# Kernel optimization log

Measured on AMD Instinct MI355X. Metric: run time of the kernel, lower is better.

Reference implementation:

```python
import jax, jax.numpy as jnp
import numpy as np

D_MODEL = 1024
NUM_HEADS = 16
D_K = D_MODEL // NUM_HEADS
EPS = 1e-12  # F.normalize eps


def setup_inputs() -> dict:
    key = jax.random.key(0)
    ks = jax.random.split(key, 12)
    B, S = 4, 2048
    scale = 1.0 / np.sqrt(D_MODEL)
    inp = {
        'query': jax.random.normal(ks[0], (B, S, D_MODEL), jnp.float32),
        'key': jax.random.normal(ks[1], (B, S, D_MODEL), jnp.float32),
        'value': jax.random.normal(ks[2], (B, S, D_MODEL), jnp.float32),
        'w_q': jax.random.normal(ks[3], (D_MODEL, D_MODEL), jnp.float32) * scale,
        'b_q': jax.random.normal(ks[4], (D_MODEL,), jnp.float32) * scale,
        'w_k': jax.random.normal(ks[5], (D_MODEL, D_MODEL), jnp.float32) * scale,
        'b_k': jax.random.normal(ks[6], (D_MODEL,), jnp.float32) * scale,
        'w_v': jax.random.normal(ks[7], (D_MODEL, D_MODEL), jnp.float32) * scale,
        'b_v': jax.random.normal(ks[8], (D_MODEL,), jnp.float32) * scale,
        'w_o': jax.random.normal(ks[9], (D_MODEL, D_MODEL), jnp.float32) * scale,
        'b_o': jax.random.normal(ks[10], (D_MODEL,), jnp.float32) * scale,
    }
    return inp


def _split_heads(x, B, S):
    # [B,S,D] -> [B,H,S,d_k]
    return x.reshape(B, S, NUM_HEADS, D_K).transpose(0, 2, 1, 3)


def _l2_normalize(x):
    # matches F.normalize(p=2, dim=-1): x / max(||x||, eps)
    n = jnp.sqrt(jnp.sum(x * x, axis=-1, keepdims=True))
    return x / jnp.maximum(n, EPS)


def reference(query, key, value, w_q, b_q, w_k, b_k, w_v, b_v, w_o, b_o):
    B, S, _ = query.shape
    Q = _split_heads(query @ w_q.T + b_q, B, S)
    K = _split_heads(key @ w_k.T + b_k, B, S)
    V = _split_heads(value @ w_v.T + b_v, B, S)
    Qn = _l2_normalize(Q)
    Kn = _l2_normalize(K)
    # cosine similarity clamped to >=1, acosh, exp(-dist)
    sim = jnp.einsum('bhqd,bhkd->bhqk', Qn, Kn)
    dist = jnp.arccosh(jnp.maximum(sim, 1.0))
    w = jnp.exp(-dist)
    out = jnp.einsum('bhqk,bhkd->bhqd', w, V)
    out = out.transpose(0, 2, 1, 3).reshape(B, S, D_MODEL)
    return out @ w_o.T + b_o
```

## Files before the change

### kernel.cpp

```cpp
#include <hip/hip_runtime.h>


constexpr int B = 4;
constexpr int S = 2048;
constexpr int D = 1024;
constexpr int SCHUNK = 32;
constexpr int NCHUNK = S / SCHUNK;

__global__ void k_colsum_partial(const float* __restrict__ value,
                                 float* __restrict__ partial) {
  const int d = blockIdx.x * blockDim.x + threadIdx.x;
  const int c = blockIdx.y;
  const int b = blockIdx.z;
  const float* p = value + (((size_t)b * S) + (size_t)c * SCHUNK) * D + d;
  float acc = 0.f;
#pragma unroll
  for (int i = 0; i < SCHUNK; ++i) acc += p[(size_t)i * D];
  partial[(((size_t)b * NCHUNK) + c) * D + d] = acc;
}

__global__ void k_colsum_reduce(const float* __restrict__ partial,
                                float* __restrict__ vsum) {
  const int d = blockIdx.x * blockDim.x + threadIdx.x;
  const int b = blockIdx.y;
  const float* p = partial + (size_t)b * NCHUNK * D + d;
  float acc = 0.f;
#pragma unroll
  for (int c = 0; c < NCHUNK; ++c) acc += p[(size_t)c * D];
  vsum[(size_t)b * D + d] = acc;
}

__global__ void k_gemv4(const float* __restrict__ x, const float* __restrict__ w,
                        const float* __restrict__ bias, float bias_scale,
                        float* __restrict__ y) {
  const int j = blockIdx.x;
  const int lane = threadIdx.x & 63;
  const int b = threadIdx.x >> 6;
  const float4* wr = (const float4*)(w + (size_t)j * D);
  const float4* xr = (const float4*)(x + (size_t)b * D);
  float acc = 0.f;
#pragma unroll
  for (int i = 0; i < D / 4 / 64; ++i) {
    float4 a = wr[lane + 64 * i];
    float4 c = xr[lane + 64 * i];
    acc += a.x * c.x + a.y * c.y + a.z * c.z + a.w * c.w;
  }
#pragma unroll
  for (int off = 32; off; off >>= 1) acc += __shfl_xor(acc, off, 64);
  if (lane == 0) y[(size_t)b * D + j] = acc + bias_scale * bias[j];
}

__global__ void k_bcast(const float* __restrict__ fin, float4* __restrict__ out) {
  const size_t idx = (size_t)blockIdx.x * blockDim.x + threadIdx.x;
  const int dp = (int)(idx & (D / 4 - 1));
  const size_t row = idx >> 8;
  const int b = (int)(row >> 11);
  out[idx] = ((const float4*)fin)[b * (D / 4) + dp];
}

extern "C" void kernel_launch(void* const* d_in, const int* in_sizes, int n_in,
                              void* d_out, int out_size, void* d_ws, size_t ws_size,
                              hipStream_t stream) {
  const float* value = (const float*)d_in[2];
  const float* w_v = (const float*)d_in[7];
  const float* b_v = (const float*)d_in[8];
  const float* w_o = (const float*)d_in[9];
  const float* b_o = (const float*)d_in[10];

  float* ws = (float*)d_ws;
  float* partial = ws;
  float* vsum = partial + (size_t)B * NCHUNK * D;
  float* attn = vsum + (size_t)B * D;
  float* fin = attn + (size_t)B * D;

  dim3 g1(D / 256, NCHUNK, B);
  k_colsum_partial<<<g1, 256, 0, stream>>>(value, partial);

  dim3 g2(D / 256, B);
  k_colsum_reduce<<<g2, 256, 0, stream>>>(partial, vsum);

  k_gemv4<<<D, 256, 0, stream>>>(vsum, w_v, b_v, (float)S, attn);
  k_gemv4<<<D, 256, 0, stream>>>(attn, w_o, b_o, 1.0f, fin);

  const size_t n4 = (size_t)B * S * D / 4;
  k_bcast<<<(unsigned)(n4 / 256), 256, 0, stream>>>(fin, (float4*)d_out);
}
```

Before: 150.3 us.

## Fuse colsum, two GEMVs and broadcast into one persistent kernel with grid barriers

Replaces five separate launches (partial column sum, reduce, two GEMVs, broadcast) with one 256-block persistent kernel. Its phases are separated by atomic-counter grid barriers, and the workspace control words are zeroed by a memset. Per-block partial sums and GEMV inputs are staged in LDS, and each wave computes one output row for all four batches. This is meant to cut launch and inter-kernel gaps. The cost is low occupancy for the bandwidth-heavy read and broadcast phases, plus a hang risk if the 256 blocks are not all co-resident.

```diff
diff --git a/kernel.cpp b/kernel.cpp
--- a/kernel.cpp
+++ b/kernel.cpp
@@ -4,84 +4,167 @@
 constexpr int B = 4;
 constexpr int S = 2048;
 constexpr int D = 1024;
-constexpr int SCHUNK = 32;
-constexpr int NCHUNK = S / SCHUNK;
+constexpr int NBLK = 256;
+constexpr int NTHR = 256;
 
-__global__ void k_colsum_partial(const float* __restrict__ value,
-                                 float* __restrict__ partial) {
-  const int d = blockIdx.x * blockDim.x + threadIdx.x;
-  const int c = blockIdx.y;
-  const int b = blockIdx.z;
-  const float* p = value + (((size_t)b * S) + (size_t)c * SCHUNK) * D + d;
-  float acc = 0.f;
-#pragma unroll
-  for (int i = 0; i < SCHUNK; ++i) acc += p[(size_t)i * D];
-  partial[(((size_t)b * NCHUNK) + c) * D + d] = acc;
+constexpr int WS_PARTIAL = 64;
+constexpr int WS_ATTN = WS_PARTIAL + 16 * 4 * 1024;
+constexpr int WS_FIN = WS_ATTN + 4096;
+
+__device__ __forceinline__ void gbarrier(unsigned* ctr, unsigned* rel) {
+  __threadfence();
+  __syncthreads();
+  if (threadIdx.x == 0) {
+    unsigned prev = __hip_atomic_fetch_add(ctr, 1u, __ATOMIC_ACQ_REL,
+                                           __HIP_MEMORY_SCOPE_AGENT);
+    if (prev == (unsigned)(NBLK - 1)) {
+      __hip_atomic_store(rel, 1u, __ATOMIC_RELEASE, __HIP_MEMORY_SCOPE_AGENT);
+    } else {
+      int spins = 0;
+      while (__hip_atomic_load(rel, __ATOMIC_ACQUIRE,
+                               __HIP_MEMORY_SCOPE_AGENT) == 0u) {
+        __builtin_amdgcn_s_sleep(2);
+        if (++spins > 30000000) break;
+      }
+    }
+  }
+  __syncthreads();
 }
 
-__global__ void k_colsum_reduce(const float* __restrict__ partial,
-                                float* __restrict__ vsum) {
-  const int d = blockIdx.x * blockDim.x + threadIdx.x;
-  const int b = blockIdx.y;
-  const float* p = partial + (size_t)b * NCHUNK * D + d;
-  float acc = 0.f;
+__global__ __launch_bounds__(NTHR, 2) void fused_hyp_attn(
+    const float4* __restrict__ value4, const float4* __restrict__ wv4,
+    const float* __restrict__ bv, const float4* __restrict__ wo4,
+    const float* __restrict__ bo, float4* __restrict__ out4,
+    float* __restrict__ ws) {
+  const int tid = threadIdx.x;
+  const int wave = tid >> 6;
+  const int lane = tid & 63;
+  const int x = blockIdx.x;
+
+  unsigned* ctrl = (unsigned*)ws;
+  float* partialv = ws + WS_PARTIAL;
+  float4* partialv4 = (float4*)partialv;
+  float* attn = ws + WS_ATTN;
+  float* fin = ws + WS_FIN;
+  const float4* fin4 = (const float4*)fin;
+
+  __shared__ float lds[4 * 1024];
+  float4* lds4 = (float4*)lds;
+
+  {
+    const int b = x & 3;
+    const int dchunk = (x >> 2) & 3;
+    const int schunk = x >> 4;
+    const int d4 = dchunk * 64 + lane;
+    const int row0 = schunk * 128 + wave * 32;
+    const float4* base = value4 + (size_t)(b * S + row0) * (D / 4) + d4;
+    float4 acc = {0.f, 0.f, 0.f, 0.f};
 #pragma unroll
-  for (int c = 0; c < NCHUNK; ++c) acc += p[(size_t)c * D];
-  vsum[(size_t)b * D + d] = acc;
-}
+    for (int i = 0; i < 32; ++i) {
+      float4 v = base[(size_t)i * (D / 4)];
+      acc.x += v.x; acc.y += v.y; acc.z += v.z; acc.w += v.w;
+    }
+    lds4[wave * 64 + lane] = acc;
+    __syncthreads();
+    if (wave == 0) {
+      float4 a0 = lds4[lane], a1 = lds4[64 + lane];
+      float4 a2 = lds4[128 + lane], a3 = lds4[192 + lane];
+      float4 s4;
+      s4.x = (a0.x + a1.x) + (a2.x + a3.x);
+      s4.y = (a0.y + a1.y) + (a2.y + a3.y);
+      s4.z = (a0.z + a1.z) + (a2.z + a3.z);
+      s4.w = (a0.w + a1.w) + (a2.w + a3.w);
+      partialv4[(schunk * 4 + b) * (D / 4) + d4] = s4;
+    }
+  }
+  gbarrier(&ctrl[0], &ctrl[8]);
 
-__global__ void k_gemv4(const float* __restrict__ x, const float* __restrict__ w,
-                        const float* __restrict__ bias, float bias_scale,
-                        float* __restrict__ y) {
-  const int j = blockIdx.x;
-  const int lane = threadIdx.x & 63;
-  const int b = threadIdx.x >> 6;
-  const float4* wr = (const float4*)(w + (size_t)j * D);
-  const float4* xr = (const float4*)(x + (size_t)b * D);
-  float acc = 0.f;
+  {
 #pragma unroll
-  for (int i = 0; i < D / 4 / 64; ++i) {
-    float4 a = wr[lane + 64 * i];
-    float4 c = xr[lane + 64 * i];
-    acc += a.x * c.x + a.y * c.y + a.z * c.z + a.w * c.w;
+    for (int i = 0; i < 16; ++i) {
+      const int idx = tid + 256 * i;
+      float s = 0.f;
+#pragma unroll
+      for (int c = 0; c < 16; ++c) s += partialv[c * 4096 + idx];
+      lds[idx] = s;
+    }
+    __syncthreads();
+    const int j = x * 4 + wave;
+    const float4* wrow = wv4 + (size_t)j * (D / 4);
+    float acc[4] = {0.f, 0.f, 0.f, 0.f};
+#pragma unroll
+    for (int it = 0; it < 4; ++it) {
+      float4 w = wrow[it * 64 + lane];
+#pragma unroll
+      for (int b = 0; b < 4; ++b) {
+        float4 xv = lds4[b * 256 + it * 64 + lane];
+        acc[b] += w.x * xv.x + w.y * xv.y + w.z * xv.z + w.w * xv.w;
+      }
+    }
+#pragma unroll
+    for (int off = 32; off; off >>= 1)
+#pragma unroll
+      for (int b = 0; b < 4; ++b) acc[b] += __shfl_xor(acc[b], off, 64);
+    if (lane == 0) {
+      const float bias = (float)S * bv[j];
+#pragma unroll
+      for (int b = 0; b < 4; ++b) attn[b * D + j] = acc[b] + bias;
+    }
   }
+  gbarrier(&ctrl[1], &ctrl[9]);
+
+  {
 #pragma unroll
-  for (int off = 32; off; off >>= 1) acc += __shfl_xor(acc, off, 64);
-  if (lane == 0) y[(size_t)b * D + j] = acc + bias_scale * bias[j];
-}
+    for (int i = 0; i < 16; ++i) {
+      const int idx = tid + 256 * i;
+      lds[idx] = attn[idx];
+    }
+    __syncthreads();
+    const int j = x * 4 + wave;
+    const float4* wrow = wo4 + (size_t)j * (D / 4);
+    float acc[4] = {0.f, 0.f, 0.f, 0.f};
+#pragma unroll
+    for (int it = 0; it < 4; ++it) {
+      float4 w = wrow[it * 64 + lane];
+#pragma unroll
+      for (int b = 0; b < 4; ++b) {
+        float4 xv = lds4[b * 256 + it * 64 + lane];
+        acc[b] += w.x * xv.x + w.y * xv.y + w.z * xv.z + w.w * xv.w;
+      }
+    }
+#pragma unroll
+    for (int off = 32; off; off >>= 1)
+#pragma unroll
+      for (int b = 0; b < 4; ++b) acc[b] += __shfl_xor(acc[b], off, 64);
+    if (lane == 0) {
+      const float bias = bo[j];
+#pragma unroll
+      for (int b = 0; b < 4; ++b) fin[b * D + j] = acc[b] + bias;
+    }
+  }
+  gbarrier(&ctrl[2], &ctrl[10]);
 
-__global__ void k_bcast(const float* __restrict__ fin, float4* __restrict__ out) {
-  const size_t idx = (size_t)blockIdx.x * blockDim.x + threadIdx.x;
-  const int dp = (int)(idx & (D / 4 - 1));
-  const size_t row = idx >> 8;
-  const int b = (int)(row >> 11);
-  out[idx] = ((const float4*)fin)[b * (D / 4) + dp];
+  {
+    const int b = x & 3;
+    const int schunk = x >> 2;
+    const float4 val = fin4[b * (D / 4) + tid];
+    const size_t rowbase = (size_t)(b * S + schunk * 32) * (D / 4) + tid;
+#pragma unroll
+    for (int r = 0; r < 32; ++r) out4[rowbase + (size_t)r * (D / 4)] = val;
+  }
 }
 
 extern "C" void kernel_launch(void* const* d_in, const int* in_sizes, int n_in,
                               void* d_out, int out_size, void* d_ws, size_t ws_size,
                               hipStream_t stream) {
-  const float* value = (const float*)d_in[2];
-  const float* w_v = (const float*)d_in[7];
-  const float* b_v = (const float*)d_in[8];
-  const float* w_o = (const float*)d_in[9];
-  const float* b_o = (const float*)d_in[10];
+  const float4* value4 = (const float4*)d_in[2];
+  const float4* wv4 = (const float4*)d_in[7];
+  const float* bv = (const float*)d_in[8];
+  const float4* wo4 = (const float4*)d_in[9];
+  const float* bo = (const float*)d_in[10];
 
-  float* ws = (float*)d_ws;
-  float* partial = ws;
-  float* vsum = partial + (size_t)B * NCHUNK * D;
-  float* attn = vsum + (size_t)B * D;
-  float* fin = attn + (size_t)B * D;
+  hipMemsetAsync(d_ws, 0, 256, stream);
 
-  dim3 g1(D / 256, NCHUNK, B);
-  k_colsum_partial<<<g1, 256, 0, stream>>>(value, partial);
-
-  dim3 g2(D / 256, B);
-  k_colsum_reduce<<<g2, 256, 0, stream>>>(partial, vsum);
-
-  k_gemv4<<<D, 256, 0, stream>>>(vsum, w_v, b_v, (float)S, attn);
-  k_gemv4<<<D, 256, 0, stream>>>(attn, w_o, b_o, 1.0f, fin);
-
-  const size_t n4 = (size_t)B * S * D / 4;
-  k_bcast<<<(unsigned)(n4 / 256), 256, 0, stream>>>(fin, (float4*)d_out);
+  fused_hyp_attn<<<NBLK, NTHR, 0, stream>>>(value4, wv4, bv, wo4, bo,
+                                            (float4*)d_out, (float*)d_ws);
 }
```

After: 258.9 us. +72.2%, slower.
